# Kernel optimization log

Measured on AMD Instinct MI355X. Metric: run time of the kernel, lower is better.

## Reference

```python
import jax, jax.numpy as jnp
import numpy as np

N = 50000      # total nodes (25 graphs x 2000 proteins)
E = 1200000    # total edges
G = 25         # graphs
F_IN = 128     # protein_features
H = 64         # hidden_dim
L = 2          # num_layers


def setup_inputs() -> dict:
    key = jax.random.key(0)
    ks = jax.random.split(key, 24)
    inp = {
        "x": jax.random.normal(ks[0], (N, F_IN), dtype=jnp.float32),
        "edge_attr": jax.random.uniform(ks[1], (E,), dtype=jnp.float32),
        "global_features": jax.random.normal(ks[2], (G, 6), dtype=jnp.float32),
        "edge_index": jax.random.randint(ks[3], (2, E), 0, N, dtype=jnp.int64),
        "batch": (jnp.arange(N, dtype=jnp.int64) // (N // G)),
    }
    s = 0.05
    inp["W_embed"] = jax.random.normal(ks[4], (F_IN, H), dtype=jnp.float32) * s
    inp["b_embed"] = jnp.zeros((H,), dtype=jnp.float32)
    inp["W_glob"] = jax.random.normal(ks[5], (6, H), dtype=jnp.float32) * s
    inp["b_glob"] = jnp.zeros((H,), dtype=jnp.float32)
    # stacked per-layer GATConv params (heads=1)
    inp["lin_W"] = jax.random.normal(ks[6], (L, H, H), dtype=jnp.float32) * s
    inp["att_src"] = jax.random.normal(ks[7], (L, H), dtype=jnp.float32) * s
    inp["att_dst"] = jax.random.normal(ks[8], (L, H), dtype=jnp.float32) * s
    inp["lin_edge_W"] = jax.random.normal(ks[9], (L, 1, H), dtype=jnp.float32) * s
    inp["att_edge"] = jax.random.normal(ks[10], (L, H), dtype=jnp.float32) * s
    inp["gat_bias"] = jnp.zeros((L, H), dtype=jnp.float32)
    inp["W_comb"] = jax.random.normal(ks[11], (2 * H, H), dtype=jnp.float32) * s
    inp["b_comb"] = jnp.zeros((H,), dtype=jnp.float32)
    inp["W_out"] = jax.random.normal(ks[12], (H, 1), dtype=jnp.float32) * s
    inp["b_out"] = jnp.zeros((1,), dtype=jnp.float32)
    return inp


def _forward(x, edge_attr, global_features, W_embed, b_embed, W_glob, b_glob,
             lin_W, att_src, att_dst, lin_edge_W, att_edge, gat_bias,
             W_comb, b_comb, W_out, b_out, edge_index, batch):
    src, dst = edge_index[0], edge_index[1]
    h = x @ W_embed + b_embed                       # [N,H]
    g = global_features @ W_glob + b_glob           # [G,H]
    ea = edge_attr[:, None]                         # [E,1] (edge_attr.unsqueeze(1))
    for l in range(L):
        hs = h @ lin_W[l]                           # [N,H] shared lin_src/lin_dst
        a_src = hs @ att_src[l]                     # [N]
        a_dst = hs @ att_dst[l]                     # [N]
        ef = ea @ lin_edge_W[l]                     # [E,H]
        a_edge = ef @ att_edge[l]                   # [E]
        alpha = jax.nn.leaky_relu(a_src[src] + a_dst[dst] + a_edge, 0.2)
        # segment softmax over incoming edges of each dst node
        m = jax.ops.segment_max(alpha, dst, num_segments=N)
        ex = jnp.exp(alpha - m[dst])
        denom = jax.ops.segment_sum(ex, dst, num_segments=N)
        alpha = ex / (denom[dst] + 1e-16)
        msg = alpha[:, None] * hs[src]              # [E,H]
        h = jax.ops.segment_sum(msg, dst, num_segments=N) + gat_bias[l]
        h = jax.nn.relu(h)
    # global_mean_pool
    counts = jax.ops.segment_sum(jnp.ones((N,), h.dtype), batch, num_segments=G)
    graph = jax.ops.segment_sum(h, batch, num_segments=G) / counts[:, None]
    combined = jax.nn.relu(jnp.concatenate([graph, g], axis=1) @ W_comb + b_comb)
    return combined @ W_out + b_out                 # [G,1]


def reference(x, edge_attr, global_features, W_embed, b_embed, W_glob, b_glob,
              lin_W, att_src, att_dst, lin_edge_W, att_edge, gat_bias,
              W_comb, b_comb, W_out, b_out, edge_index, batch):
    return _forward(x, edge_attr, global_features, W_embed, b_embed, W_glob, b_glob,
                    lin_W, att_src, att_dst, lin_edge_W, att_edge, gat_bias,
                    W_comb, b_comb, W_out, b_out, edge_index, batch)
```

## Files before the change

kernel.cpp:

```cpp
#include <hip/hip_runtime.h>
#include <hip/hip_fp16.h>
#include <math.h>

#define N_NODES 50000
#define N_EDGES 1200000
#define N_GRAPH 25
#define F_IN 128
#define H_DIM 64
#define NODES_PER_GRAPH 2000

#define NBUCK 196
#define BUCK_CAP 8000
#define EPB 4096
#define NB_BIN ((N_EDGES + EPB - 1) / EPB)
#define NB_GEMM ((N_NODES + 63) / 64)

#define OFF_H     0
#define OFF_HS    (N_NODES*64)
#define OFF_ASRC  (OFF_HS + N_NODES*64)
#define OFF_ADST  (OFF_ASRC + N_NODES)
#define OFF_CBUF  (OFF_ADST + N_NODES)
#define OFF_BCUR  (OFF_CBUF + 16)
#define OFF_GSUM  (OFF_BCUR + 256)
#define OFF_ROWP  (OFF_GSUM + N_GRAPH*64)
#define OFF_ESRT  (OFF_ROWP + N_NODES + 2)
#define OFF_EL2   (OFF_ESRT + N_EDGES)
#define OFF_STAGE (OFF_EL2 + 2*N_EDGES)

__global__ __launch_bounds__(256) void k_embed(const float* __restrict__ x,
                                               const float* __restrict__ W,
                                               const float* __restrict__ b,
                                               float* __restrict__ h,
                                               const float* __restrict__ linE,
                                               const float* __restrict__ attE,
                                               float* __restrict__ cbuf,
                                               int* __restrict__ bcur,
                                               float* __restrict__ gsum) {
    __shared__ float4 sW4[F_IN * 16];
    __shared__ float4 sx4[64 * 17];
    int tid = threadIdx.x;
    if (blockIdx.x == 0) {
        for (int i = tid; i < 256; i += 256) bcur[i] = 0;
        for (int i = tid; i < N_GRAPH * 64; i += 256) gsum[i] = 0.f;
        if (tid < 128) {
            int l = tid >> 6, j = tid & 63;
            float v = linE[l * 64 + j] * attE[l * 64 + j];
            #pragma unroll
            for (int m = 1; m < 64; m <<= 1) v += __shfl_xor(v, m);
            if (j == 0) cbuf[l] = v;
        }
    }
    int n0 = blockIdx.x * 64;
    const float4* W4 = (const float4*)W;
    const float4* x4 = (const float4*)x;
    #pragma unroll
    for (int i = 0; i < 8; ++i) sW4[tid + i * 256] = W4[tid + i * 256];

    int c4 = tid & 15, ng = tid >> 4;
    int r = tid >> 4, q = tid & 15;
    float4 acc[4];
    #pragma unroll
    for (int j = 0; j < 4; ++j) acc[j] = make_float4(0.f, 0.f, 0.f, 0.f);

    for (int kh = 0; kh < 2; ++kh) {
        __syncthreads();
        #pragma unroll
        for (int rb = 0; rb < 4; ++rb) {
            int rr = r + rb * 16;
            int n = n0 + rr;
            float4 v = make_float4(0.f, 0.f, 0.f, 0.f);
            if (n < N_NODES) v = x4[(size_t)n * 32 + kh * 16 + q];
            sx4[rr * 17 + q] = v;
        }
        __syncthreads();
        #pragma unroll
        for (int kq = 0; kq < 16; ++kq) {
            float4 wv[4];
            #pragma unroll
            for (int kk = 0; kk < 4; ++kk) wv[kk] = sW4[(kh * 64 + kq * 4 + kk) * 16 + c4];
            #pragma unroll
            for (int j = 0; j < 4; ++j) {
                float4 xv = sx4[(ng * 4 + j) * 17 + kq];
                float xs[4] = {xv.x, xv.y, xv.z, xv.w};
                #pragma unroll
                for (int kk = 0; kk < 4; ++kk) {
                    acc[j].x = fmaf(xs[kk], wv[kk].x, acc[j].x);
                    acc[j].y = fmaf(xs[kk], wv[kk].y, acc[j].y);
                    acc[j].z = fmaf(xs[kk], wv[kk].z, acc[j].z);
                    acc[j].w = fmaf(xs[kk], wv[kk].w, acc[j].w);
                }
            }
        }
    }
    float4 bb = ((const float4*)b)[c4];
    #pragma unroll
    for (int j = 0; j < 4; ++j) {
        int n = n0 + ng * 4 + j;
        if (n < N_NODES) {
            float4 v;
            v.x = acc[j].x + bb.x; v.y = acc[j].y + bb.y;
            v.z = acc[j].z + bb.z; v.w = acc[j].w + bb.w;
            ((float4*)h)[(size_t)n * 16 + c4] = v;
        }
    }
}

__global__ __launch_bounds__(256) void k_hs(const float* __restrict__ hin,
                                            const float* __restrict__ W,
                                            const float* __restrict__ attS,
                                            const float* __restrict__ attD,
                                            __half* __restrict__ hs_h,
                                            float* __restrict__ asrc,
                                            float* __restrict__ adst) {
    __shared__ float4 sW4[H_DIM * 16];
    __shared__ float4 sx4[64 * 17];
    int tid = threadIdx.x;
    int n0 = blockIdx.x * 64;
    const float4* W4 = (const float4*)W;
    const float4* h4 = (const float4*)hin;
    #pragma unroll
    for (int i = 0; i < 4; ++i) sW4[tid + i * 256] = W4[tid + i * 256];
    int r = tid >> 4, q = tid & 15;
    #pragma unroll
    for (int rb = 0; rb < 4; ++rb) {
        int rr = r + rb * 16;
        int n = n0 + rr;
        float4 v = make_float4(0.f, 0.f, 0.f, 0.f);
        if (n < N_NODES) v = h4[(size_t)n * 16 + q];
        sx4[rr * 17 + q] = v;
    }
    __syncthreads();

    int c4 = tid & 15, ng = tid >> 4;
    float4 acc[4];
    #pragma unroll
    for (int j = 0; j < 4; ++j) acc[j] = make_float4(0.f, 0.f, 0.f, 0.f);
    #pragma unroll
    for (int kq = 0; kq < 16; ++kq) {
        float4 wv[4];
        #pragma unroll
        for (int kk = 0; kk < 4; ++kk) wv[kk] = sW4[(kq * 4 + kk) * 16 + c4];
        #pragma unroll
        for (int j = 0; j < 4; ++j) {
            float4 xv = sx4[(ng * 4 + j) * 17 + kq];
            float xs[4] = {xv.x, xv.y, xv.z, xv.w};
            #pragma unroll
            for (int kk = 0; kk < 4; ++kk) {
                acc[j].x = fmaf(xs[kk], wv[kk].x, acc[j].x);
                acc[j].y = fmaf(xs[kk], wv[kk].y, acc[j].y);
                acc[j].z = fmaf(xs[kk], wv[kk].z, acc[j].z);
                acc[j].w = fmaf(xs[kk], wv[kk].w, acc[j].w);
            }
        }
    }
    float4 aS = ((const float4*)attS)[c4];
    float4 aD = ((const float4*)attD)[c4];
    #pragma unroll
    for (int j = 0; j < 4; ++j) {
        int n = n0 + ng * 4 + j;
        float rs = acc[j].x * aS.x + acc[j].y * aS.y + acc[j].z * aS.z + acc[j].w * aS.w;
        float rd = acc[j].x * aD.x + acc[j].y * aD.y + acc[j].z * aD.z + acc[j].w * aD.w;
        #pragma unroll
        for (int o = 1; o < 16; o <<= 1) {
            rs += __shfl_xor(rs, o);
            rd += __shfl_xor(rd, o);
        }
        if (n < N_NODES) {
            __half2 p0 = __floats2half2_rn(acc[j].x, acc[j].y);
            __half2 p1 = __floats2half2_rn(acc[j].z, acc[j].w);
            uint2 st;
            st.x = *(unsigned*)&p0;
            st.y = *(unsigned*)&p1;
            ((uint2*)hs_h)[(size_t)n * 16 + c4] = st;
            if (c4 == 0) { asrc[n] = rs; adst[n] = rd; }
        }
    }
}

__global__ __launch_bounds__(256) void k_el(const unsigned* __restrict__ esrt,
                                            const float* __restrict__ asrc,
                                            const float* __restrict__ cbuf,
                                            int layer,
                                            uint2* __restrict__ el2) {
    int e = blockIdx.x * 256 + threadIdx.x;
    if (e >= N_EDGES) return;
    unsigned v = esrt[e];
    unsigned s = v & 0xFFFFu;
    float eav = __uint_as_float(v & 0xFFFF0000u);
    float lg = asrc[s] + cbuf[layer] * eav;
    uint2 r; r.x = __float_as_uint(lg); r.y = s;
    el2[e] = r;
}

__device__ __forceinline__ int block_excl_scan(int v, int tid, int* lds, int* total) {
    int lane = tid & 63, w = tid >> 6;
    int incl = v;
    #pragma unroll
    for (int off = 1; off < 64; off <<= 1) {
        int t = __shfl_up(incl, off);
        if (lane >= off) incl += t;
    }
    if (lane == 63) lds[w] = incl;
    __syncthreads();
    int wo = 0;
    for (int i = 0; i < w; ++i) wo += lds[i];
    *total = lds[0] + lds[1] + lds[2] + lds[3];
    __syncthreads();
    return wo + incl - v;
}

__global__ __launch_bounds__(256) void k_bin(const int* __restrict__ ei,
                                             const float* __restrict__ ea,
                                             uint2* __restrict__ stage,
                                             int* __restrict__ bcur) {
    __shared__ int lcnt[NBUCK];
    __shared__ int lbase[NBUCK];
    int tid = threadIdx.x;
    for (int i = tid; i < NBUCK; i += 256) lcnt[i] = 0;
    __syncthreads();
    int e0 = blockIdx.x * EPB;
    unsigned pw0[16], pw1[16];
    #pragma unroll
    for (int k = 0; k < 16; ++k) {
        int e = e0 + k * 256 + tid;
        bool ok = e < N_EDGES;
        int s = ok ? ei[e] : 0;
        int d = ok ? ei[N_EDGES + e] : 0;
        float v = ok ? ea[e] : 0.f;
        pw0[k] = (unsigned)s | ((unsigned)d << 16);
        pw1[k] = __float_as_uint(v);
        if (ok) atomicAdd(&lcnt[d >> 8], 1);
    }
    __syncthreads();
    for (int i = tid; i < NBUCK; i += 256) {
        lbase[i] = atomicAdd(&bcur[i], lcnt[i]);
        lcnt[i] = 0;
    }
    __syncthreads();
    #pragma unroll
    for (int k = 0; k < 16; ++k) {
        int e = e0 + k * 256 + tid;
        if (e < N_EDGES) {
            int b = pw0[k] >> 24;
            int pos = lbase[b] + atomicAdd(&lcnt[b], 1);
            uint2 t; t.x = pw0[k]; t.y = pw1[k];
            stage[b * BUCK_CAP + pos] = t;
        }
    }
}

__global__ __launch_bounds__(256) void k_group(const uint2* __restrict__ stage,
                                               const int* __restrict__ bcur,
                                               int* __restrict__ rowp,
                                               unsigned* __restrict__ esrt,
                                               const float* __restrict__ asrc,
                                               const float* __restrict__ cbuf,
                                               uint2* __restrict__ el2) {
    int b = blockIdx.x;
    int tid = threadIdx.x;
    __shared__ int sprefix[256];
    __shared__ int lcnt[256];
    __shared__ int lofs[256];
    __shared__ int slds[4];
    int bv = (tid < NBUCK) ? bcur[tid] : 0;
    int total;
    int bex = block_excl_scan(bv, tid, slds, &total);
    sprefix[tid] = bex;
    lcnt[tid] = 0;
    __syncthreads();
    int base = sprefix[b];
    int cntb = bcur[b];
    float c0 = cbuf[0];
    const uint2* reg = stage + b * BUCK_CAP;
    for (int i = tid; i < cntb; i += 256)
        atomicAdd(&lcnt[(reg[i].x >> 16) & 255], 1);
    __syncthreads();
    int ex = block_excl_scan(lcnt[tid], tid, slds, &total);
    lofs[tid] = base + ex;
    int n = b * 256 + tid;
    if (n < N_NODES) rowp[n] = base + ex;
    if (b == 0 && tid == 0) rowp[N_NODES] = N_EDGES;
    __syncthreads();
    lcnt[tid] = 0;
    __syncthreads();
    for (int i = tid; i < cntb; i += 256) {
        uint2 v = reg[i];
        int dloc = (v.x >> 16) & 255;
        int pos = lofs[dloc] + atomicAdd(&lcnt[dloc], 1);
        unsigned s = v.x & 0xFFFFu;
        unsigned eab = (v.y + 0x8000u) & 0xFFFF0000u;
        esrt[pos] = s | eab;
        float lg = asrc[s] + c0 * __uint_as_float(eab);
        uint2 r; r.x = __float_as_uint(lg); r.y = s;
        el2[pos] = r;
    }
}

template <bool POOL>
__global__ __launch_bounds__(256) void k_fused(const int* __restrict__ rowp,
                                               const uint2* __restrict__ el2,
                                               const float* __restrict__ adst,
                                               const __half* __restrict__ hs_h,
                                               int layer,
                                               const float* __restrict__ gbias,
                                               float* __restrict__ hout,
                                               float* __restrict__ gsum) {
    __shared__ float sblock[64];
    int tid = threadIdx.x;
    if (POOL) {
        if (tid < 64) sblock[tid] = 0.f;
        __syncthreads();
    }
    int pair = (blockIdx.x * 256 + tid) >> 6;
    int lane = tid & 63;
    int half = lane >> 5, l32 = lane & 31;
    int wid = pair * 2 + half;
    if (wid < N_NODES) {
        int beg = rowp[wid], end = rowp[wid + 1];
        float adv = adst[wid];
        float psum = 0.f;
        float acc[8];
        #pragma unroll
        for (int j = 0; j < 8; ++j) acc[j] = 0.f;
        int g = (lane >> 3) & 3;
        int fl8 = lane & 7;
        int hb = half * 32;
        const uint4* hsq = (const uint4*)hs_h;

#define UNPACK_FMA(w_, r_)                                                      \
        {                                                                       \
            __half2 h0_ = *(__half2*)&r_.x, h1_ = *(__half2*)&r_.y;             \
            __half2 h2_ = *(__half2*)&r_.z, h3_ = *(__half2*)&r_.w;             \
            float2 f0_ = __half22float2(h0_), f1_ = __half22float2(h1_);        \
            float2 f2_ = __half22float2(h2_), f3_ = __half22float2(h3_);        \
            acc[0] = fmaf(w_, f0_.x, acc[0]); acc[1] = fmaf(w_, f0_.y, acc[1]); \
            acc[2] = fmaf(w_, f1_.x, acc[2]); acc[3] = fmaf(w_, f1_.y, acc[3]); \
            acc[4] = fmaf(w_, f2_.x, acc[4]); acc[5] = fmaf(w_, f2_.y, acc[5]); \
            acc[6] = fmaf(w_, f3_.x, acc[6]); acc[7] = fmaf(w_, f3_.y, acc[7]); \
        }

        for (int base = beg; base < end; base += 32) {
            int idx = base + l32;
            bool ok = idx < end;
            float exv = 0.f;
            int s = 0;
            if (ok) {
                uint2 v = el2[idx];
                s = (int)v.y;
                float a = __uint_as_float(v.x) + adv;
                a = a >= 0.f ? a : 0.2f * a;
                exv = __expf(a);
            }
            psum += exv;

            int lim = end - base; if (lim > 32) lim = 32;
            int t = g;
            for (; t + 12 < lim; t += 16) {
                float w0 = __shfl(exv, hb + t),      w1 = __shfl(exv, hb + t + 4);
                float w2 = __shfl(exv, hb + t + 8),  w3 = __shfl(exv, hb + t + 12);
                int   s0 = __shfl(s, hb + t),        s1 = __shfl(s, hb + t + 4);
                int   s2 = __shfl(s, hb + t + 8),    s3 = __shfl(s, hb + t + 12);
                uint4 r0 = hsq[s0 * 8 + fl8];
                uint4 r1 = hsq[s1 * 8 + fl8];
                uint4 r2 = hsq[s2 * 8 + fl8];
                uint4 r3 = hsq[s3 * 8 + fl8];
                UNPACK_FMA(w0, r0);
                UNPACK_FMA(w1, r1);
                UNPACK_FMA(w2, r2);
                UNPACK_FMA(w3, r3);
            }
            for (; t < lim; t += 4) {
                float w0 = __shfl(exv, hb + t);
                int   s0 = __shfl(s, hb + t);
                uint4 r0 = hsq[s0 * 8 + fl8];
                UNPACK_FMA(w0, r0);
            }
        }
#undef UNPACK_FMA
        #pragma unroll
        for (int o = 1; o < 32; o <<= 1) psum += __shfl_xor(psum, o);
        #pragma unroll
        for (int o = 8; o < 32; o <<= 1) {
            #pragma unroll
            for (int j = 0; j < 8; ++j) acc[j] += __shfl_xor(acc[j], o);
        }

        if (l32 < 8) {
            float inv = 1.f / (psum + 1e-16f);
            const float* gb = gbias + layer * H_DIM + l32 * 8;
            float vals[8];
            #pragma unroll
            for (int j = 0; j < 8; ++j) {
                float v = acc[j] * inv + gb[j];
                vals[j] = v > 0.f ? v : 0.f;
            }
            if (POOL) {
                #pragma unroll
                for (int j = 0; j < 8; ++j)
                    atomicAdd(&sblock[l32 * 8 + j], vals[j]);
            } else {
                float* op = hout + (size_t)wid * H_DIM + l32 * 8;
                float4 v0 = make_float4(vals[0], vals[1], vals[2], vals[3]);
                float4 v1 = make_float4(vals[4], vals[5], vals[6], vals[7]);
                ((float4*)op)[0] = v0;
                ((float4*)op)[1] = v1;
            }
        }
    }
    if (POOL) {
        __syncthreads();
        int gg = (blockIdx.x * 8) / NODES_PER_GRAPH;
        if (tid < 64) atomicAdd(gsum + gg * H_DIM + tid, sblock[tid]);
    }
}

__global__ __launch_bounds__(64) void k_head2(const float* __restrict__ gsum,
                                              const float* __restrict__ gf,
                                              const float* __restrict__ Wg,
                                              const float* __restrict__ bg,
                                              const float* __restrict__ Wc,
                                              const float* __restrict__ bc,
                                              const float* __restrict__ Wo,
                                              const float* __restrict__ bo,
                                              float* __restrict__ out) {
    int g = blockIdx.x;
    int lane = threadIdx.x;
    __shared__ float sgraph[64];
    __shared__ float sgf[64];
    sgraph[lane] = gsum[g * H_DIM + lane] / (float)NODES_PER_GRAPH;
    float gv = bg[lane];
    #pragma unroll
    for (int k = 0; k < 6; ++k) gv += gf[g * 6 + k] * Wg[k * 64 + lane];
    sgf[lane] = gv;
    __syncthreads();
    float cj = bc[lane];
    #pragma unroll
    for (int k = 0; k < 64; ++k) cj += sgraph[k] * Wc[k * 64 + lane];
    #pragma unroll
    for (int k = 0; k < 64; ++k) cj += sgf[k] * Wc[(64 + k) * 64 + lane];
    cj = cj > 0.f ? cj : 0.f;
    float o = cj * Wo[lane];
    #pragma unroll
    for (int m = 1; m < 64; m <<= 1) o += __shfl_xor(o, m);
    if (lane == 0) out[g] = o + bo[0];
}

extern "C" void kernel_launch(void* const* d_in, const int* in_sizes, int n_in,
                              void* d_out, int out_size, void* d_ws, size_t ws_size,
                              hipStream_t stream) {
    const float* x        = (const float*)d_in[0];
    const float* ea       = (const float*)d_in[1];
    const float* gf       = (const float*)d_in[2];
    const int*   ei       = (const int*)d_in[3];
    const float* W_embed  = (const float*)d_in[5];
    const float* b_embed  = (const float*)d_in[6];
    const float* W_glob   = (const float*)d_in[7];
    const float* b_glob   = (const float*)d_in[8];
    const float* lin_W    = (const float*)d_in[9];
    const float* att_src  = (const float*)d_in[10];
    const float* att_dst  = (const float*)d_in[11];
    const float* lin_eW   = (const float*)d_in[12];
    const float* att_edge = (const float*)d_in[13];
    const float* gat_bias = (const float*)d_in[14];
    const float* W_comb   = (const float*)d_in[15];
    const float* b_comb   = (const float*)d_in[16];
    const float* W_out    = (const float*)d_in[17];
    const float* b_out    = (const float*)d_in[18];
    float* out = (float*)d_out;
    float* ws  = (float*)d_ws;

    float*    h      = ws + OFF_H;
    __half*   hs_h   = (__half*)(ws + OFF_HS);
    float*    asrc   = ws + OFF_ASRC;
    float*    adst   = ws + OFF_ADST;
    float*    cbuf   = ws + OFF_CBUF;
    int*      bcur   = (int*)(ws + OFF_BCUR);
    float*    gsum   = ws + OFF_GSUM;
    int*      rowp   = (int*)(ws + OFF_ROWP);
    unsigned* esrt   = (unsigned*)(ws + OFF_ESRT);
    uint2*    el2    = (uint2*)(ws + OFF_EL2);
    uint2*    stage  = (uint2*)(ws + OFF_STAGE);

    const int egrid = (N_EDGES + 255) / 256;
    const int fgrid = N_NODES / 8;

    k_embed<<<NB_GEMM, 256, 0, stream>>>(x, W_embed, b_embed, h,
                                         lin_eW, att_edge, cbuf, bcur, gsum);
    k_hs<<<NB_GEMM, 256, 0, stream>>>(h, lin_W,
                                      att_src, att_dst, hs_h, asrc, adst);

    k_bin<<<NB_BIN, 256, 0, stream>>>(ei, ea, stage, bcur);
    k_group<<<NBUCK, 256, 0, stream>>>(stage, bcur, rowp, esrt, asrc, cbuf, el2);

    k_fused<false><<<fgrid, 256, 0, stream>>>(rowp, el2, adst, hs_h, 0,
                                              gat_bias, h, gsum);
    k_hs<<<NB_GEMM, 256, 0, stream>>>(h, lin_W + 64 * 64,
                                      att_src + 64, att_dst + 64, hs_h, asrc, adst);
    k_el<<<egrid, 256, 0, stream>>>(esrt, asrc, cbuf, 1, el2);
    k_fused<true><<<fgrid, 256, 0, stream>>>(rowp, el2, adst, hs_h, 1,
                                             gat_bias, h, gsum);

    k_head2<<<N_GRAPH, 64, 0, stream>>>(gsum, gf, W_glob, b_glob,
                                        W_comb, b_comb, W_out, b_out, out);
}
```

Before: 199.6 us.

## Drop precomputed edge-logit array and merge hs GEMM with edge binning kernel

Removes the per-edge el2 logit buffer and the k_el kernel. The fused aggregation kernel now reads the packed esrt word and gathers asrc[s] itself to compute the logit inline. The first hs GEMM and the edge-binning pass are merged into one launch that splits work by block index, so the two independent tasks can share the device. This cuts two launches and the 8-byte-per-edge write and read, at the cost of an extra random gather of asrc inside the softmax loop and larger shared memory for the bin blocks.

```diff
diff --git a/kernel.cpp b/kernel.cpp
--- a/kernel.cpp
+++ b/kernel.cpp
@@ -24,8 +24,7 @@
 #define OFF_GSUM  (OFF_BCUR + 256)
 #define OFF_ROWP  (OFF_GSUM + N_GRAPH*64)
 #define OFF_ESRT  (OFF_ROWP + N_NODES + 2)
-#define OFF_EL2   (OFF_ESRT + N_EDGES)
-#define OFF_STAGE (OFF_EL2 + 2*N_EDGES)
+#define OFF_STAGE (OFF_ESRT + N_EDGES)
 
 __global__ __launch_bounds__(256) void k_embed(const float* __restrict__ x,
                                                const float* __restrict__ W,
@@ -105,17 +104,16 @@
     }
 }
 
-__global__ __launch_bounds__(256) void k_hs(const float* __restrict__ hin,
-                                            const float* __restrict__ W,
-                                            const float* __restrict__ attS,
-                                            const float* __restrict__ attD,
-                                            __half* __restrict__ hs_h,
-                                            float* __restrict__ asrc,
-                                            float* __restrict__ adst) {
-    __shared__ float4 sW4[H_DIM * 16];
-    __shared__ float4 sx4[64 * 17];
-    int tid = threadIdx.x;
-    int n0 = blockIdx.x * 64;
+__device__ __forceinline__ void hs_body(int n0, char* smem, int tid,
+                                        const float* __restrict__ hin,
+                                        const float* __restrict__ W,
+                                        const float* __restrict__ attS,
+                                        const float* __restrict__ attD,
+                                        __half* __restrict__ hs_h,
+                                        float* __restrict__ asrc,
+                                        float* __restrict__ adst) {
+    float4* sW4 = (float4*)smem;
+    float4* sx4 = (float4*)(smem + 16384);
     const float4* W4 = (const float4*)W;
     const float4* h4 = (const float4*)hin;
     #pragma unroll
@@ -177,48 +175,28 @@
     }
 }
 
-__global__ __launch_bounds__(256) void k_el(const unsigned* __restrict__ esrt,
-                                            const float* __restrict__ asrc,
-                                            const float* __restrict__ cbuf,
-                                            int layer,
-                                            uint2* __restrict__ el2) {
-    int e = blockIdx.x * 256 + threadIdx.x;
-    if (e >= N_EDGES) return;
-    unsigned v = esrt[e];
-    unsigned s = v & 0xFFFFu;
-    float eav = __uint_as_float(v & 0xFFFF0000u);
-    float lg = asrc[s] + cbuf[layer] * eav;
-    uint2 r; r.x = __float_as_uint(lg); r.y = s;
-    el2[e] = r;
-}
-
-__device__ __forceinline__ int block_excl_scan(int v, int tid, int* lds, int* total) {
-    int lane = tid & 63, w = tid >> 6;
-    int incl = v;
-    #pragma unroll
-    for (int off = 1; off < 64; off <<= 1) {
-        int t = __shfl_up(incl, off);
-        if (lane >= off) incl += t;
-    }
-    if (lane == 63) lds[w] = incl;
-    __syncthreads();
-    int wo = 0;
-    for (int i = 0; i < w; ++i) wo += lds[i];
-    *total = lds[0] + lds[1] + lds[2] + lds[3];
-    __syncthreads();
-    return wo + incl - v;
-}
-
-__global__ __launch_bounds__(256) void k_bin(const int* __restrict__ ei,
-                                             const float* __restrict__ ea,
-                                             uint2* __restrict__ stage,
-                                             int* __restrict__ bcur) {
-    __shared__ int lcnt[NBUCK];
-    __shared__ int lbase[NBUCK];
+__global__ __launch_bounds__(256) void k_hs_bin(const float* __restrict__ hin,
+                                                const float* __restrict__ W,
+                                                const float* __restrict__ attS,
+                                                const float* __restrict__ attD,
+                                                __half* __restrict__ hs_h,
+                                                float* __restrict__ asrc,
+                                                float* __restrict__ adst,
+                                                const int* __restrict__ ei,
+                                                const float* __restrict__ ea,
+                                                uint2* __restrict__ stage,
+                                                int* __restrict__ bcur) {
+    __shared__ __align__(16) char smem[33792];
     int tid = threadIdx.x;
+    if (blockIdx.x < NB_GEMM) {
+        hs_body(blockIdx.x * 64, smem, tid, hin, W, attS, attD, hs_h, asrc, adst);
+        return;
+    }
+    int* lcnt  = (int*)smem;
+    int* lbase = (int*)(smem + 1024);
     for (int i = tid; i < NBUCK; i += 256) lcnt[i] = 0;
     __syncthreads();
-    int e0 = blockIdx.x * EPB;
+    int e0 = (blockIdx.x - NB_GEMM) * EPB;
     unsigned pw0[16], pw1[16];
     #pragma unroll
     for (int k = 0; k < 16; ++k) {
@@ -249,13 +227,38 @@
     }
 }
 
+__global__ __launch_bounds__(256) void k_hs(const float* __restrict__ hin,
+                                            const float* __restrict__ W,
+                                            const float* __restrict__ attS,
+                                            const float* __restrict__ attD,
+                                            __half* __restrict__ hs_h,
+                                            float* __restrict__ asrc,
+                                            float* __restrict__ adst) {
+    __shared__ __align__(16) char smem[33792];
+    hs_body(blockIdx.x * 64, smem, threadIdx.x, hin, W, attS, attD, hs_h, asrc, adst);
+}
+
+__device__ __forceinline__ int block_excl_scan(int v, int tid, int* lds, int* total) {
+    int lane = tid & 63, w = tid >> 6;
+    int incl = v;
+    #pragma unroll
+    for (int off = 1; off < 64; off <<= 1) {
+        int t = __shfl_up(incl, off);
+        if (lane >= off) incl += t;
+    }
+    if (lane == 63) lds[w] = incl;
+    __syncthreads();
+    int wo = 0;
+    for (int i = 0; i < w; ++i) wo += lds[i];
+    *total = lds[0] + lds[1] + lds[2] + lds[3];
+    __syncthreads();
+    return wo + incl - v;
+}
+
 __global__ __launch_bounds__(256) void k_group(const uint2* __restrict__ stage,
                                                const int* __restrict__ bcur,
                                                int* __restrict__ rowp,
-                                               unsigned* __restrict__ esrt,
-                                               const float* __restrict__ asrc,
-                                               const float* __restrict__ cbuf,
-                                               uint2* __restrict__ el2) {
+                                               unsigned* __restrict__ esrt) {
     int b = blockIdx.x;
     int tid = threadIdx.x;
     __shared__ int sprefix[256];
@@ -270,7 +273,6 @@
     __syncthreads();
     int base = sprefix[b];
     int cntb = bcur[b];
-    float c0 = cbuf[0];
     const uint2* reg = stage + b * BUCK_CAP;
     for (int i = tid; i < cntb; i += 256)
         atomicAdd(&lcnt[(reg[i].x >> 16) & 255], 1);
@@ -287,20 +289,17 @@
         uint2 v = reg[i];
         int dloc = (v.x >> 16) & 255;
         int pos = lofs[dloc] + atomicAdd(&lcnt[dloc], 1);
-        unsigned s = v.x & 0xFFFFu;
-        unsigned eab = (v.y + 0x8000u) & 0xFFFF0000u;
-        esrt[pos] = s | eab;
-        float lg = asrc[s] + c0 * __uint_as_float(eab);
-        uint2 r; r.x = __float_as_uint(lg); r.y = s;
-        el2[pos] = r;
+        esrt[pos] = (v.x & 0xFFFFu) | ((v.y + 0x8000u) & 0xFFFF0000u);
     }
 }
 
 template <bool POOL>
 __global__ __launch_bounds__(256) void k_fused(const int* __restrict__ rowp,
-                                               const uint2* __restrict__ el2,
+                                               const unsigned* __restrict__ esrt,
+                                               const float* __restrict__ asrc,
                                                const float* __restrict__ adst,
                                                const __half* __restrict__ hs_h,
+                                               const float* __restrict__ cbuf,
                                                int layer,
                                                const float* __restrict__ gbias,
                                                float* __restrict__ hout,
@@ -318,6 +317,7 @@
     if (wid < N_NODES) {
         int beg = rowp[wid], end = rowp[wid + 1];
         float adv = adst[wid];
+        float c = cbuf[layer];
         float psum = 0.f;
         float acc[8];
         #pragma unroll
@@ -345,9 +345,10 @@
             float exv = 0.f;
             int s = 0;
             if (ok) {
-                uint2 v = el2[idx];
-                s = (int)v.y;
-                float a = __uint_as_float(v.x) + adv;
+                unsigned v = esrt[idx];
+                s = (int)(v & 0xFFFFu);
+                float eav = __uint_as_float(v & 0xFFFF0000u);
+                float a = asrc[s] + c * eav + adv;
                 a = a >= 0.f ? a : 0.2f * a;
                 exv = __expf(a);
             }
@@ -478,28 +479,22 @@
     float*    gsum   = ws + OFF_GSUM;
     int*      rowp   = (int*)(ws + OFF_ROWP);
     unsigned* esrt   = (unsigned*)(ws + OFF_ESRT);
-    uint2*    el2    = (uint2*)(ws + OFF_EL2);
     uint2*    stage  = (uint2*)(ws + OFF_STAGE);
 
-    const int egrid = (N_EDGES + 255) / 256;
     const int fgrid = N_NODES / 8;
 
     k_embed<<<NB_GEMM, 256, 0, stream>>>(x, W_embed, b_embed, h,
                                          lin_eW, att_edge, cbuf, bcur, gsum);
-    k_hs<<<NB_GEMM, 256, 0, stream>>>(h, lin_W,
-                                      att_src, att_dst, hs_h, asrc, adst);
-
-    k_bin<<<NB_BIN, 256, 0, stream>>>(ei, ea, stage, bcur);
-    k_group<<<NBUCK, 256, 0, stream>>>(stage, bcur, rowp, esrt, asrc, cbuf, el2);
-
-    k_fused<false><<<fgrid, 256, 0, stream>>>(rowp, el2, adst, hs_h, 0,
+    k_hs_bin<<<NB_GEMM + NB_BIN, 256, 0, stream>>>(h, lin_W,
+                                                   att_src, att_dst, hs_h, asrc, adst,
+                                                   ei, ea, stage, bcur);
+    k_group<<<NBUCK, 256, 0, stream>>>(stage, bcur, rowp, esrt);
+    k_fused<false><<<fgrid, 256, 0, stream>>>(rowp, esrt, asrc, adst, hs_h, cbuf, 0,
                                               gat_bias, h, gsum);
     k_hs<<<NB_GEMM, 256, 0, stream>>>(h, lin_W + 64 * 64,
                                       att_src + 64, att_dst + 64, hs_h, asrc, adst);
-    k_el<<<egrid, 256, 0, stream>>>(esrt, asrc, cbuf, 1, el2);
-    k_fused<true><<<fgrid, 256, 0, stream>>>(rowp, el2, adst, hs_h, 1,
+    k_fused<true><<<fgrid, 256, 0, stream>>>(rowp, esrt, asrc, adst, hs_h, cbuf, 1,
                                              gat_bias, h, gsum);
-
     k_head2<<<N_GRAPH, 64, 0, stream>>>(gsum, gf, W_glob, b_glob,
                                         W_comb, b_comb, W_out, b_out, out);
 }
```

New measurement: 184.5 us. 7.6% less time.
